# Kernel optimization log

Measured on AMD Instinct MI355X. Metric: run time of the kernel, lower is better.

## Reference

```python
import jax, jax.numpy as jnp
import numpy as np

B, S, D, H, L = 16, 1024, 512, 8, 3
NUM_Q, NUM_C, TOTAL_RES = 10000, 300, 2


def setup_inputs() -> dict:
    k = jax.random.split(jax.random.key(0), 20)
    n = lambda i, s, sc=0.02: jax.random.normal(k[i], s, jnp.float32) * sc
    z = lambda: jnp.zeros((D,), jnp.float32)
    o = lambda: jnp.ones((D,), jnp.float32)
    return {
        'in_ex': jax.random.randint(k[0], (B, S), 0, NUM_Q),
        'in_cat': jax.random.randint(k[1], (B, S), 0, NUM_C),
        'in_res': jax.random.randint(k[2], (B, S), 0, 2),
        'in_pos': n(3, (B, S, D)),
        'en_out': n(4, (B, S, D)),
        'E_res': n(5, (TOTAL_RES + 1, D)),
        'E_ex': n(6, (2 * NUM_Q + 1, D)),
        'E_cat': n(7, (2 * NUM_C + 1, D)),
        'g1': o(), 'be1': z(), 'g2': o(), 'be2': z(), 'g3': o(), 'be3': z(),
        'Wq1': n(8, (D, D)), 'bq1': z(), 'Wk1': n(9, (D, D)), 'bk1': z(),
        'Wv1': n(10, (D, D)), 'bv1': z(), 'Wo1': n(11, (D, D)), 'bo1': z(),
        'Wq2': n(12, (D, D)), 'bq2': z(), 'Wk2': n(13, (D, D)), 'bk2': z(),
        'Wv2': n(14, (D, D)), 'bv2': z(), 'Wo2': n(15, (D, D)), 'bo2': z(),
        'fW1': n(16, (D, D)), 'fb1': z(), 'fW2': n(17, (D, D)), 'fb2': z(),
    }


def layer_norm(x, g, b, eps=1e-5):
    m = x.mean(-1, keepdims=True)
    v = ((x - m) ** 2).mean(-1, keepdims=True)
    return (x - m) / jnp.sqrt(v + eps) * g + b


def pyr_attn(q_in, kv_in, Wq, bq, Wk, bk, Wv, bv, Wo, bo):
    # q_in, kv_in: (S, B, D) as in nn.MultiheadAttention convention
    Sq, Bq, Dm = q_in.shape
    dh = Dm // H
    heads = lambda x: x.reshape(x.shape[0], Bq, H, dh).transpose(1, 2, 0, 3)  # (B,H,S,dh)
    qh = heads(q_in @ Wq + bq)
    kh = heads(kv_in @ Wk + bk)
    vh = heads(kv_in @ Wv + bv)
    Skv = kv_in.shape[0]
    i = jnp.arange(Sq)[:, None]
    Ks, Vs, Ms = [], [], []
    for l in range(L):  # pyramid levels: keys/values avg-pooled by 2**l
        f = 2 ** l
        nb = Skv // f
        Ks.append(kh[:, :, :nb * f].reshape(Bq, H, nb, f, dh).mean(3))
        Vs.append(vh[:, :, :nb * f].reshape(Bq, H, nb, f, dh).mean(3))
        # causal: query i may attend pooled block j only if the block ends at or before i
        Ms.append(i >= (jnp.arange(nb)[None, :] + 1) * f - 1)
    K = jnp.concatenate(Ks, 2)
    V = jnp.concatenate(Vs, 2)
    M = jnp.concatenate(Ms, 1)  # (Sq, K_total) multi-level causal mask
    sc = jnp.einsum('bhqd,bhkd->bhqk', qh, K) / np.sqrt(dh).astype(np.float32)
    sc = jnp.where(M[None, None], sc, -1e9)
    a = jax.nn.softmax(sc, -1)
    out = jnp.einsum('bhqk,bhkd->bhqd', a, V)
    return out.transpose(2, 0, 1, 3).reshape(Sq, Bq, Dm) @ Wo + bo


def reference(in_ex, in_cat, in_res, in_pos, en_out, E_res, E_ex, E_cat,
              g1, be1, g2, be2, g3, be3,
              Wq1, bq1, Wk1, bk1, Wv1, bv1, Wo1, bo1,
              Wq2, bq2, Wk2, bk2, Wv2, bv2, Wo2, bo2,
              fW1, fb1, fW2, fb2):
    # embedding sum (first_block=True)
    out = E_res[in_res] + E_ex[in_ex + NUM_Q * in_res] + E_cat[in_cat + NUM_C * in_res] + in_pos
    out = out.transpose(1, 0, 2)  # (S, B, D)
    out = layer_norm(out, g1, be1)
    out = out + pyr_attn(out, out, Wq1, bq1, Wk1, bk1, Wv1, bv1, Wo1, bo1)
    en = layer_norm(en_out.transpose(1, 0, 2), g2, be2)
    out = out + pyr_attn(out, en, Wq2, bq2, Wk2, bk2, Wv2, bv2, Wo2, bo2)
    out = out.transpose(1, 0, 2)  # (B, S, D)
    out = layer_norm(out, g3, be3)
    out = out + (jax.nn.relu(out @ fW1 + fb1) @ fW2 + fb2)
    return out
```

## Files before the change

### kernel.cpp

```cpp
#include <hip/hip_runtime.h>


#define BB 16
#define SS 1024
#define DD 512
#define HH 8
#define DH 64
#define KTOT 1792
#define NROW (BB*SS)
#define KSW 80

typedef unsigned short u16;
typedef __attribute__((ext_vector_type(8))) u16 u16x8;
typedef __attribute__((ext_vector_type(4))) u16 u16x4;
typedef __attribute__((ext_vector_type(8))) short s16x8;
typedef __attribute__((ext_vector_type(4))) float f32x4;

__device__ __forceinline__ float b2f(u16 u) {
    return __uint_as_float(((unsigned int)u) << 16);
}
__device__ __forceinline__ u16 f2b(float f) {
    unsigned int u = __float_as_uint(f);
    return (u16)((u + 0x7FFF + ((u >> 16) & 1)) >> 16);
}
__device__ __forceinline__ s16x8 u2s8(u16x8 u) {
    union { u16x8 u; s16x8 s; } x; x.u = u; return x.s;
}
__device__ __forceinline__ f32x4 mfma16(s16x8 a, s16x8 b, f32x4 c) {
    return __builtin_amdgcn_mfma_f32_16x16x32_bf16(a, b, c, 0, 0, 0);
}
__device__ __forceinline__ float wave_sum(float v) {
    #pragma unroll
    for (int m = 1; m < 64; m <<= 1) v += __shfl_xor(v, m, 64);
    return v;
}
__device__ __forceinline__ float exp2a(float x) {
    float r;
    asm("v_exp_f32 %0, %1" : "=v"(r) : "v"(x));
    return r;
}
__device__ __forceinline__ unsigned int cvtpk(float a, float b) {
    unsigned int r;
    asm("v_cvt_pk_bf16_f32 %0, %1, %2" : "=v"(r) : "v"(a), "v"(b));
    return r;
}
__device__ __forceinline__ void gl16(const void* g, void* l) {
    __builtin_amdgcn_global_load_lds(
        (const __attribute__((address_space(1))) void*)(unsigned long long)g,
        (__attribute__((address_space(3))) void*)(unsigned int)(unsigned long long)l,
        16, 0, 0);
}

__global__ __launch_bounds__(256) void embed_ln_k(
    const int* __restrict__ in_ex, const int* __restrict__ in_cat,
    const int* __restrict__ in_res, const float* __restrict__ in_pos,
    const float* __restrict__ E_res, const float* __restrict__ E_ex,
    const float* __restrict__ E_cat, const float* __restrict__ g,
    const float* __restrict__ be, float* __restrict__ out)
{
    int wave = threadIdx.x >> 6, lane = threadIdx.x & 63;
    int row = blockIdx.x * 4 + wave;
    int res = in_res[row];
    int ex  = in_ex[row] + 10000 * res;
    int cat = in_cat[row] + 300 * res;
    int d0 = lane * 8;
    const float* pr = &E_res[(size_t)res * DD + d0];
    const float* pe = &E_ex[(size_t)ex * DD + d0];
    const float* pc = &E_cat[(size_t)cat * DD + d0];
    const float* pp = &in_pos[(size_t)row * DD + d0];
    float x[8]; float s = 0.f;
    #pragma unroll
    for (int j = 0; j < 8; j++) { x[j] = pr[j] + pe[j] + pc[j] + pp[j]; s += x[j]; }
    s = wave_sum(s);
    float mean = s * (1.0f / DD);
    float vs = 0.f;
    #pragma unroll
    for (int j = 0; j < 8; j++) { float d = x[j] - mean; vs += d * d; }
    vs = wave_sum(vs);
    float rstd = rsqrtf(vs * (1.0f / DD) + 1e-5f);
    #pragma unroll
    for (int j = 0; j < 8; j++)
        out[(size_t)row * DD + d0 + j] = (x[j] - mean) * rstd * g[d0 + j] + be[d0 + j];
}

template<bool OUTB>
__global__ __launch_bounds__(256) void ln_k(
    const float* __restrict__ x, const float* __restrict__ g,
    const float* __restrict__ be, void* __restrict__ outv)
{
    int wave = threadIdx.x >> 6, lane = threadIdx.x & 63;
    int row = blockIdx.x * 4 + wave;
    int d0 = lane * 8;
    const float* px = &x[(size_t)row * DD + d0];
    float xv[8]; float s = 0.f;
    #pragma unroll
    for (int j = 0; j < 8; j++) { xv[j] = px[j]; s += xv[j]; }
    s = wave_sum(s);
    float mean = s * (1.0f / DD);
    float vs = 0.f;
    #pragma unroll
    for (int j = 0; j < 8; j++) { float d = xv[j] - mean; vs += d * d; }
    vs = wave_sum(vs);
    float rstd = rsqrtf(vs * (1.0f / DD) + 1e-5f);
    #pragma unroll
    for (int j = 0; j < 8; j++) {
        float v = (xv[j] - mean) * rstd * g[d0 + j] + be[d0 + j];
        if (OUTB) ((u16*)outv)[(size_t)row * DD + d0 + j] = f2b(v);
        else      ((float*)outv)[(size_t)row * DD + d0 + j] = v;
    }
}

__global__ __launch_bounds__(256) void transpose_k(const float* __restrict__ src, u16* __restrict__ dst)
{
    int idx = blockIdx.x * 256 + threadIdx.x;
    int n = idx & 511, k = idx >> 9;
    dst[n * 512 + k] = f2b(src[k * 512 + n]);
}

__global__ __launch_bounds__(256) void pool_k12_k(u16* __restrict__ KP)
{
    int idx = blockIdx.x * 256 + threadIdx.x;
    int d = idx & 63;
    int t = idx >> 6;
    int k12 = t % 768;
    int bh = t / 768;
    int s0, f;
    if (k12 < 512) { s0 = 2 * k12; f = 2; } else { s0 = 4 * (k12 - 512); f = 4; }
    size_t base = (size_t)bh * KTOT * DH;
    float acc = 0.f;
    for (int i = 0; i < f; i++)
        acc += b2f(KP[base + (size_t)(s0 + i) * DH + d]);
    KP[base + (size_t)(1024 + k12) * DH + d] = f2b(acc * (1.0f / (float)f));
}

__global__ __launch_bounds__(256) void pool_vt_k(const u16* __restrict__ Vp, u16* __restrict__ VPt)
{
    __shared__ __align__(16) u16 T[64 * 72];
    int tid = threadIdx.x;
    int st = blockIdx.x;
    int h  = blockIdx.y;
    int b  = blockIdx.z;
    int s0 = st * 64;
    {
        const u16* src = &Vp[((size_t)(b * SS + s0)) * DD + h * DH];
        #pragma unroll
        for (int it = 0; it < 2; it++) {
            int idx = it * 256 + tid;
            int row = idx >> 3, unit = idx & 7;
            *(u16x8*)&T[row * 72 + unit * 8] =
                *(const u16x8*)&src[(size_t)row * DD + unit * 8];
        }
    }
    __syncthreads();
    int d = tid & 63, g = tid >> 6;
    size_t obase = ((size_t)(b * HH + h) * DH + d) * KTOT;
    #pragma unroll
    for (int gg = 0; gg < 2; gg++) {
        int grp = g * 2 + gg;
        u16x8 v;
        #pragma unroll
        for (int j = 0; j < 8; j++) v[j] = T[(grp * 8 + j) * 72 + d];
        *(u16x8*)&VPt[obase + s0 + grp * 8] = v;
    }
    {
        u16x8 v;
        #pragma unroll
        for (int j = 0; j < 8; j++) {
            int sl = g * 8 + j;
            float a = b2f(T[(2 * sl) * 72 + d]) + b2f(T[(2 * sl + 1) * 72 + d]);
            v[j] = f2b(a * 0.5f);
        }
        *(u16x8*)&VPt[obase + 1024 + st * 32 + g * 8] = v;
    }
    {
        u16x4 v;
        #pragma unroll
        for (int j = 0; j < 4; j++) {
            int s2 = g * 4 + j;
            float a = 0.f;
            #pragma unroll
            for (int i = 0; i < 4; i++) a += b2f(T[(4 * s2 + i) * 72 + d]);
            v[j] = f2b(a * 0.25f);
        }
        *(u16x4*)&VPt[obase + 1536 + st * 16 + g * 4] = v;
    }
}

template<bool AF32, bool RELU, bool RES, bool OUTB, bool KLAY>
__global__ __launch_bounds__(256) void gemm_k(
    const void* __restrict__ Av, const u16* __restrict__ Wt,
    const float* __restrict__ bias, const float* __restrict__ resid,
    void* __restrict__ Cv, int M, int K, float oscale)
{
    const int N = 512;
    constexpr int ASW = AF32 ? 40 : 32;
    __shared__ __align__(16) u16 As[2][128 * ASW];
    __shared__ __align__(16) u16 Bs[2][128 * 32];
    int tid = threadIdx.x;
    int wave = tid >> 6, lane = tid & 63;
    int quad = lane >> 4, l16 = lane & 15;
    int m0 = blockIdx.y * 128, n0 = blockIdx.x * 128;
    int wm = (wave >> 1) * 64, wn = (wave & 1) * 64;
    int r = tid >> 1, cg = (tid & 1) * 16;
    int grow = wave * 16 + (lane >> 2);
    int gk = (lane & 3) * 8;
    const float* Af = (const float*)Av;
    const u16*  Ab = (const u16*)Av;
    f32x4 acc[4][4];
    #pragma unroll
    for (int i = 0; i < 4; i++)
        #pragma unroll
        for (int j = 0; j < 4; j++)
            #pragma unroll
            for (int rr = 0; rr < 4; rr++) acc[i][j][rr] = 0.f;

    const int NT = K >> 5;
    f32x4 s0, s1, s2, s3;

    #define ISSUE_B(t, buf) { int k0_ = (t) << 5; \
        gl16(&Wt[(size_t)(n0 + grow) * 512 + k0_ + gk],      &Bs[buf][grow * 32 + gk]); \
        gl16(&Wt[(size_t)(n0 + 64 + grow) * 512 + k0_ + gk], &Bs[buf][(64 + grow) * 32 + gk]); }
    #define ISSUE_A16(t, buf) { int k0_ = (t) << 5; \
        gl16(&Ab[(size_t)(m0 + grow) * K + k0_ + gk],      &As[buf][grow * 32 + gk]); \
        gl16(&Ab[(size_t)(m0 + 64 + grow) * K + k0_ + gk], &As[buf][(64 + grow) * 32 + gk]); }
    #define LOAD_A32(t) { const float* src_ = &Af[(size_t)(m0 + r) * K + ((t) << 5) + cg]; \
        s0 = *(const f32x4*)&src_[0];  s1 = *(const f32x4*)&src_[4]; \
        s2 = *(const f32x4*)&src_[8];  s3 = *(const f32x4*)&src_[12]; }
    #define WRITE_A32(buf) { union { unsigned int w[4]; u16x8 v; } L_, H_; \
        L_.w[0] = cvtpk(s0[0], s0[1]); L_.w[1] = cvtpk(s0[2], s0[3]); \
        L_.w[2] = cvtpk(s1[0], s1[1]); L_.w[3] = cvtpk(s1[2], s1[3]); \
        H_.w[0] = cvtpk(s2[0], s2[1]); H_.w[1] = cvtpk(s2[2], s2[3]); \
        H_.w[2] = cvtpk(s3[0], s3[1]); H_.w[3] = cvtpk(s3[2], s3[3]); \
        *(u16x8*)&As[buf][r * ASW + cg]     = L_.v; \
        *(u16x8*)&As[buf][r * ASW + cg + 8] = H_.v; }

    if (AF32) { LOAD_A32(0); WRITE_A32(0); }
    else      { ISSUE_A16(0, 0); }
    ISSUE_B(0, 0);
    __syncthreads();

    for (int t = 0; t < NT; ++t) {
        int cur = t & 1, nxt = cur ^ 1;
        if (t + 1 < NT) {
            if (AF32) { LOAD_A32(t + 1); }
            else      { ISSUE_A16(t + 1, nxt); }
            ISSUE_B(t + 1, nxt);
        }
        s16x8 af[4], bfr[4];
        #pragma unroll
        for (int i = 0; i < 4; i++)
            af[i] = u2s8(*(const u16x8*)&As[cur][(wm + i * 16 + l16) * ASW + quad * 8]);
        #pragma unroll
        for (int j = 0; j < 4; j++)
            bfr[j] = u2s8(*(const u16x8*)&Bs[cur][(wn + j * 16 + l16) * 32 + quad * 8]);
        #pragma unroll
        for (int i = 0; i < 4; i++)
            #pragma unroll
            for (int j = 0; j < 4; j++)
                acc[i][j] = mfma16(af[i], bfr[j], acc[i][j]);
        if (AF32 && t + 1 < NT) { WRITE_A32(nxt); }
        __syncthreads();
    }
    #undef ISSUE_B
    #undef ISSUE_A16
    #undef LOAD_A32
    #undef WRITE_A32

    #pragma unroll
    for (int j = 0; j < 4; j++) {
        int col = n0 + wn + j * 16 + l16;
        float bv = bias[col];
        #pragma unroll
        for (int i = 0; i < 4; i++) {
            int rowb = m0 + wm + i * 16 + quad * 4;
            #pragma unroll
            for (int rr = 0; rr < 4; rr++) {
                float v = (acc[i][j][rr] + bv) * oscale;
                if (RELU) v = fmaxf(v, 0.f);
                int row = rowb + rr;
                if (RES) v += resid[(size_t)row * N + col];
                if (KLAY) {
                    int b_ = row >> 10, s_ = row & 1023;
                    size_t dst = (((size_t)(b_ * HH + (col >> 6)) * KTOT) + s_) * DH + (col & 63);
                    ((u16*)Cv)[dst] = f2b(v);
                } else if (OUTB) {
                    ((u16*)Cv)[(size_t)row * N + col] = f2b(v);
                } else {
                    ((float*)Cv)[(size_t)row * N + col] = v;
                }
            }
        }
    }
}

__global__ __launch_bounds__(256, 2) void attn_k(
    const u16* __restrict__ Qp, const u16* __restrict__ KP,
    const u16* __restrict__ VPt, u16* __restrict__ Hout)
{
    __shared__ __align__(16) u16 Ksh[2][64 * KSW];
    __shared__ __align__(16) u16 Vsh[2][64 * KSW];
    int tid = threadIdx.x;
    int wave = tid >> 6, lane = tid & 63;
    int quad = lane >> 4, l16 = lane & 15;
    int id = blockIdx.x;
    int h = id & 7;
    int inner = id >> 3;
    int x = inner & 3, b = inner >> 2;

    int wx = x * 4 + wave;
    int tiles[4] = { wx, 31 - wx, 32 + wx, 63 - wx };

    const u16* Kb = KP  + ((size_t)(b * HH + h)) * KTOT * DH;
    const u16* Vt = VPt + ((size_t)(b * HH + h)) * DH * KTOT;

    s16x8 qa[4][2];
    f32x4 o[4][4];
    float lrun[4];
    int q0a[4];
    #pragma unroll
    for (int c = 0; c < 4; c++) {
        int q0 = tiles[c] * 16;
        q0a[c] = q0;
        lrun[c] = 0.f;
        const u16* qrow = Qp + ((size_t)(b * SS + q0 + l16)) * DD + h * DH;
        qa[c][0] = u2s8(*(const u16x8*)&qrow[quad * 8]);
        qa[c][1] = u2s8(*(const u16x8*)&qrow[32 + quad * 8]);
        #pragma unroll
        for (int j = 0; j < 4; j++)
            #pragma unroll
            for (int rr = 0; rr < 4; rr++) o[c][j][rr] = 0.f;
    }

    int row0 = 8 * (l16 >> 2) + (l16 & 3);

    int u0 = tid, u1 = 256 + tid;
    int kr0 = u0 >> 3, ku0 = (u0 & 7) * 8;
    int kr1 = u1 >> 3, ku1 = (u1 & 7) * 8;

    u16x8 kreg0 = *(const u16x8*)&Kb[(size_t)u0 * 8];
    u16x8 kreg1 = *(const u16x8*)&Kb[(size_t)u1 * 8];
    u16x8 vreg0 = *(const u16x8*)&Vt[(size_t)kr0 * KTOT + ku0];
    u16x8 vreg1 = *(const u16x8*)&Vt[(size_t)kr1 * KTOT + ku1];
    *(u16x8*)&Ksh[0][kr0 * KSW + ku0] = kreg0;
    *(u16x8*)&Ksh[0][kr1 * KSW + ku1] = kreg1;
    *(u16x8*)&Vsh[0][kr0 * KSW + ku0] = vreg0;
    *(u16x8*)&Vsh[0][kr1 * KSW + ku1] = vreg1;
    __syncthreads();

    for (int ch = 0; ch < 28; ch++) {
        int cur = ch & 1;
        int kbase = ch * 64;
        int lv = (ch < 16) ? 0 : (ch < 24) ? 1 : 2;
        if (ch + 1 < 28) {
            int nb = (ch + 1) * 64;
            kreg0 = *(const u16x8*)&Kb[(size_t)nb * DH + u0 * 8];
            kreg1 = *(const u16x8*)&Kb[(size_t)nb * DH + u1 * 8];
            vreg0 = *(const u16x8*)&Vt[(size_t)kr0 * KTOT + nb + ku0];
            vreg1 = *(const u16x8*)&Vt[(size_t)kr1 * KTOT + nb + ku1];
        }

        int efirst = (lv == 0) ? kbase
                   : (lv == 1) ? 2 * (kbase - 1024) + 1
                               : 4 * (kbase - 1536) + 3;
        int elast  = (lv == 0) ? kbase + 63
                   : (lv == 1) ? 2 * (kbase + 63 - 1024) + 1
                               : 4 * (kbase + 63 - 1536) + 3;
        bool act[4];
        #pragma unroll
        for (int c = 0; c < 4; c++) act[c] = (efirst <= q0a[c] + 15);

        if (act[0] | act[1] | act[2] | act[3]) {
            s16x8 fA[4], fB[4];
            #pragma unroll
            for (int t = 0; t < 4; t++) {
                const int toff = (t & 1) * 4 + (t >> 1) * 32;
                const u16* kr = &Ksh[cur][(row0 + toff) * KSW];
                fA[t] = u2s8(*(const u16x8*)&kr[quad * 8]);
                fB[t] = u2s8(*(const u16x8*)&kr[32 + quad * 8]);
            }
            s16x8 pfa[4], pfb[4];
            #pragma unroll
            for (int c = 0; c < 4; c++) {
                if (!act[c]) continue;
                f32x4 zt[4];
                __builtin_amdgcn_s_setprio(1);
                #pragma unroll
                for (int t = 0; t < 4; t++) {
                    f32x4 z;
                    #pragma unroll
                    for (int rr = 0; rr < 4; rr++) z[rr] = 0.f;
                    z = mfma16(fA[t], qa[c][0], z);
                    zt[t] = mfma16(fB[t], qa[c][1], z);
                }
                __builtin_amdgcn_s_setprio(0);

                if (elast > q0a[c]) {
                    int q = q0a[c] + l16;
                    int kmaxv = (lv == 0) ? q - kbase
                              : (lv == 1) ? ((q - 1) >> 1) - (kbase - 1024)
                                          : ((q - 3) >> 2) - (kbase - 1536);
                    int thrb = kmaxv - 8 * quad;
                    #pragma unroll
                    for (int t = 0; t < 4; t++) {
                        int thr = thrb - ((t & 1) * 4 + (t >> 1) * 32);
                        #pragma unroll
                        for (int rr = 0; rr < 4; rr++)
                            if (rr > thr) zt[t][rr] = -1e30f;
                    }
                }

                float p[4][4]; float ps0 = 0.f, ps1 = 0.f;
                #pragma unroll
                for (int t = 0; t < 4; t++)
                    #pragma unroll
                    for (int rr = 0; rr < 4; rr++) {
                        p[t][rr] = exp2a(zt[t][rr]);
                        if (t & 1) ps1 += p[t][rr]; else ps0 += p[t][rr];
                    }
                float ps = ps0 + ps1;
                ps += __shfl_xor(ps, 16, 64);
                ps += __shfl_xor(ps, 32, 64);
                lrun[c] += ps;

                union { unsigned int w[4]; u16x8 v; } U0, U1;
                U0.w[0] = cvtpk(p[0][0], p[0][1]); U0.w[1] = cvtpk(p[0][2], p[0][3]);
                U0.w[2] = cvtpk(p[1][0], p[1][1]); U0.w[3] = cvtpk(p[1][2], p[1][3]);
                U1.w[0] = cvtpk(p[2][0], p[2][1]); U1.w[1] = cvtpk(p[2][2], p[2][3]);
                U1.w[2] = cvtpk(p[3][0], p[3][1]); U1.w[3] = cvtpk(p[3][2], p[3][3]);
                pfa[c] = u2s8(U0.v); pfb[c] = u2s8(U1.v);
            }

            s16x8 vA[4], vB[4];
            #pragma unroll
            for (int j = 0; j < 4; j++) {
                const u16* vr = &Vsh[cur][(j * 16 + l16) * KSW];
                vA[j] = u2s8(*(const u16x8*)&vr[quad * 8]);
                vB[j] = u2s8(*(const u16x8*)&vr[32 + quad * 8]);
            }
            __builtin_amdgcn_s_setprio(1);
            #pragma unroll
            for (int c = 0; c < 4; c++) {
                if (!act[c]) continue;
                #pragma unroll
                for (int j = 0; j < 4; j++) {
                    o[c][j] = mfma16(pfa[c], vA[j], o[c][j]);
                    o[c][j] = mfma16(pfb[c], vB[j], o[c][j]);
                }
            }
            __builtin_amdgcn_s_setprio(0);
        }

        if (ch + 1 < 28) {
            int nxt = cur ^ 1;
            *(u16x8*)&Ksh[nxt][kr0 * KSW + ku0] = kreg0;
            *(u16x8*)&Ksh[nxt][kr1 * KSW + ku1] = kreg1;
            *(u16x8*)&Vsh[nxt][kr0 * KSW + ku0] = vreg0;
            *(u16x8*)&Vsh[nxt][kr1 * KSW + ku1] = vreg1;
        }
        __syncthreads();
    }

    #pragma unroll
    for (int c = 0; c < 4; c++) {
        float il = 1.0f / lrun[c];
        float ilr[4];
        #pragma unroll
        for (int rr = 0; rr < 4; rr++) ilr[rr] = __shfl(il, quad * 4 + rr, 64);
        #pragma unroll
        for (int rr = 0; rr < 4; rr++) {
            int q = q0a[c] + quad * 4 + rr;
            #pragma unroll
            for (int j = 0; j < 4; j++)
                Hout[((size_t)(b * SS + q)) * DD + h * DH + j * 16 + l16] = f2b(o[c][j][rr] * ilr[rr]);
        }
    }
}

extern "C" void kernel_launch(void* const* d_in, const int* in_sizes, int n_in,
                              void* d_out, int out_size, void* d_ws, size_t ws_size,
                              hipStream_t stream)
{
    (void)in_sizes; (void)n_in; (void)out_size; (void)ws_size;
    const int* in_ex  = (const int*)d_in[0];
    const int* in_cat = (const int*)d_in[1];
    const int* in_res = (const int*)d_in[2];
    const float* in_pos = (const float*)d_in[3];
    const float* en_out = (const float*)d_in[4];
    const float* E_res  = (const float*)d_in[5];
    const float* E_ex   = (const float*)d_in[6];
    const float* E_cat  = (const float*)d_in[7];
    const float* g1 = (const float*)d_in[8],  *be1 = (const float*)d_in[9];
    const float* g2 = (const float*)d_in[10], *be2 = (const float*)d_in[11];
    const float* g3 = (const float*)d_in[12], *be3 = (const float*)d_in[13];
    const float* Wq1 = (const float*)d_in[14], *bq1 = (const float*)d_in[15];
    const float* Wk1 = (const float*)d_in[16], *bk1 = (const float*)d_in[17];
    const float* Wv1 = (const float*)d_in[18], *bv1 = (const float*)d_in[19];
    const float* Wo1 = (const float*)d_in[20], *bo1 = (const float*)d_in[21];
    const float* Wq2 = (const float*)d_in[22], *bq2 = (const float*)d_in[23];
    const float* Wk2 = (const float*)d_in[24], *bk2 = (const float*)d_in[25];
    const float* Wv2 = (const float*)d_in[26], *bv2 = (const float*)d_in[27];
    const float* Wo2 = (const float*)d_in[28], *bo2 = (const float*)d_in[29];
    const float* fW1 = (const float*)d_in[30], *fb1 = (const float*)d_in[31];
    const float* fW2 = (const float*)d_in[32], *fb2 = (const float*)d_in[33];

    char* ws = (char*)d_ws;
    const size_t U = (size_t)NROW * DD * 2;
    float* x1 = (float*)(ws);
    u16* qb   = (u16*)(ws + 2 * U);
    u16* vb   = (u16*)(ws + 3 * U);
    u16* hb   = (u16*)(ws + 4 * U);
    u16* kp   = (u16*)(ws + 5 * U);
    u16* vpt  = (u16*)(ws + 5 * U + 7 * U / 4);
    u16* wt   = (u16*)(ws + 8 * U + U / 2);
    float* x2 = (float*)d_out;
    u16* en = (u16*)(ws);
    float* x3 = x1;
    float* x4 = (float*)(ws + 5 * U);
    u16* ff1 = hb;

    const float* wsrc[10] = {Wq1, Wk1, Wv1, Wo1, Wq2, Wk2, Wv2, Wo2, fW1, fW2};
    for (int i = 0; i < 10; i++)
        transpose_k<<<1024, 256, 0, stream>>>(wsrc[i], wt + (size_t)i * 262144);
    u16* tWq1 = wt,            *tWk1 = wt + 262144,   *tWv1 = wt + 2*262144, *tWo1 = wt + 3*262144;
    u16* tWq2 = wt + 4*262144, *tWk2 = wt + 5*262144, *tWv2 = wt + 6*262144, *tWo2 = wt + 7*262144;
    u16* tF1  = wt + 8*262144, *tF2  = wt + 9*262144;

    dim3 ggrid(4, 128);
    dim3 vtgrid(16, 8, 16);
    const float QSC = 0.18033688f;

    embed_ln_k<<<4096, 256, 0, stream>>>(in_ex, in_cat, in_res, in_pos,
                                         E_res, E_ex, E_cat, g1, be1, x1);

    gemm_k<true,false,false,true,false><<<ggrid, 256, 0, stream>>>(x1, tWq1, bq1, nullptr, qb, NROW, 512, QSC);
    gemm_k<true,false,false,true,true ><<<ggrid, 256, 0, stream>>>(x1, tWk1, bk1, nullptr, kp, NROW, 512, 1.0f);
    gemm_k<true,false,false,true,false><<<ggrid, 256, 0, stream>>>(x1, tWv1, bv1, nullptr, vb, NROW, 512, 1.0f);
    pool_k12_k<<<24576, 256, 0, stream>>>(kp);
    pool_vt_k<<<vtgrid, 256, 0, stream>>>(vb, vpt);
    attn_k<<<512, 256, 0, stream>>>(qb, kp, vpt, hb);
    gemm_k<false,false,true,false,false><<<ggrid, 256, 0, stream>>>(hb, tWo1, bo1, x1, x2, NROW, 512, 1.0f);

    ln_k<true><<<4096, 256, 0, stream>>>(en_out, g2, be2, en);
    gemm_k<true,false,false,true,false><<<ggrid, 256, 0, stream>>>(x2, tWq2, bq2, nullptr, qb, NROW, 512, QSC);
    gemm_k<false,false,false,true,true ><<<ggrid, 256, 0, stream>>>(en, tWk2, bk2, nullptr, kp, NROW, 512, 1.0f);
    gemm_k<false,false,false,true,false><<<ggrid, 256, 0, stream>>>(en, tWv2, bv2, nullptr, vb, NROW, 512, 1.0f);
    pool_k12_k<<<24576, 256, 0, stream>>>(kp);
    pool_vt_k<<<vtgrid, 256, 0, stream>>>(vb, vpt);
    attn_k<<<512, 256, 0, stream>>>(qb, kp, vpt, hb);
    gemm_k<false,false,true,false,false><<<ggrid, 256, 0, stream>>>(hb, tWo2, bo2, x2, x3, NROW, 512, 1.0f);

    ln_k<false><<<4096, 256, 0, stream>>>(x3, g3, be3, x4);
    gemm_k<true,true,false,true,false><<<ggrid, 256, 0, stream>>>(x4, tF1, fb1, nullptr, ff1, NROW, 512, 1.0f);
    gemm_k<false,false,true,false,false><<<ggrid, 256, 0, stream>>>(ff1, tF2, fb2, x4, (float*)d_out, NROW, 512, 1.0f);
}
```

Before: 642.3 us.

## Fuse K pooling into GEMM epilogue, batch weight transposes, split attention finer

The K-projection GEMM epilogue now writes the level-1 and level-2 pooled key rows directly from its four consecutive accumulator rows, which removes the separate pool_k12_k pass (two launches and a re-read of K). The ten per-weight transpose launches become one tiled, LDS-staged transpose kernel that uses vectorized loads and stores. Attention blocks now cover two query tiles per wave instead of four, with double the grid and launch bounds raised to 4 blocks per SM. This improves parallelism and balance but halves K/V tile reuse per block load.

```diff
diff --git a/kernel.cpp b/kernel.cpp
--- a/kernel.cpp
+++ b/kernel.cpp
@@ -110,27 +110,42 @@
     }
 }
 
-__global__ __launch_bounds__(256) void transpose_k(const float* __restrict__ src, u16* __restrict__ dst)
-{
-    int idx = blockIdx.x * 256 + threadIdx.x;
-    int n = idx & 511, k = idx >> 9;
-    dst[n * 512 + k] = f2b(src[k * 512 + n]);
-}
-
-__global__ __launch_bounds__(256) void pool_k12_k(u16* __restrict__ KP)
-{
-    int idx = blockIdx.x * 256 + threadIdx.x;
-    int d = idx & 63;
-    int t = idx >> 6;
-    int k12 = t % 768;
-    int bh = t / 768;
-    int s0, f;
-    if (k12 < 512) { s0 = 2 * k12; f = 2; } else { s0 = 4 * (k12 - 512); f = 4; }
-    size_t base = (size_t)bh * KTOT * DH;
-    float acc = 0.f;
-    for (int i = 0; i < f; i++)
-        acc += b2f(KP[base + (size_t)(s0 + i) * DH + d]);
-    KP[base + (size_t)(1024 + k12) * DH + d] = f2b(acc * (1.0f / (float)f));
+struct W10 { const float* p[10]; };
+__global__ __launch_bounds__(256) void transpose_all_k(W10 wp, u16* __restrict__ dst)
+{
+    __shared__ __align__(16) u16 T[64 * 72];
+    int w = blockIdx.z;
+    const float* src = wp.p[w];
+    u16* d = dst + (size_t)w * 262144;
+    int tk = blockIdx.x;
+    int tn = blockIdx.y;
+    int tid = threadIdx.x;
+    {
+        int r = tid >> 4;
+        int c4 = (tid & 15) * 4;
+        #pragma unroll
+        for (int it = 0; it < 4; it++) {
+            int kr = it * 16 + r;
+            const float* s4 = &src[(size_t)(tk * 64 + kr) * 512 + tn * 64 + c4];
+            f32x4 v = *(const f32x4*)s4;
+            *(unsigned int*)&T[kr * 72 + c4]     = cvtpk(v[0], v[1]);
+            *(unsigned int*)&T[kr * 72 + c4 + 2] = cvtpk(v[2], v[3]);
+        }
+    }
+    __syncthreads();
+    {
+        int nn = tid >> 2;
+        int k16 = (tid & 3) * 16;
+        u16x8 a, b;
+        #pragma unroll
+        for (int j = 0; j < 8; j++) {
+            a[j] = T[(k16 + j) * 72 + nn];
+            b[j] = T[(k16 + 8 + j) * 72 + nn];
+        }
+        u16* o = &d[(size_t)(tn * 64 + nn) * 512 + tk * 64 + k16];
+        *(u16x8*)&o[0] = a;
+        *(u16x8*)&o[8] = b;
+    }
 }
 
 __global__ __launch_bounds__(256) void pool_vt_k(const u16* __restrict__ Vp, u16* __restrict__ VPt)
@@ -273,27 +288,36 @@
         #pragma unroll
         for (int i = 0; i < 4; i++) {
             int rowb = m0 + wm + i * 16 + quad * 4;
-            #pragma unroll
-            for (int rr = 0; rr < 4; rr++) {
-                float v = (acc[i][j][rr] + bv) * oscale;
-                if (RELU) v = fmaxf(v, 0.f);
-                int row = rowb + rr;
-                if (RES) v += resid[(size_t)row * N + col];
-                if (KLAY) {
-                    int b_ = row >> 10, s_ = row & 1023;
-                    size_t dst = (((size_t)(b_ * HH + (col >> 6)) * KTOT) + s_) * DH + (col & 63);
-                    ((u16*)Cv)[dst] = f2b(v);
-                } else if (OUTB) {
-                    ((u16*)Cv)[(size_t)row * N + col] = f2b(v);
-                } else {
-                    ((float*)Cv)[(size_t)row * N + col] = v;
+            if (KLAY) {
+                float vv[4];
+                #pragma unroll
+                for (int rr = 0; rr < 4; rr++) vv[rr] = acc[i][j][rr] + bv;
+                int b_ = rowb >> 10, s_ = rowb & 1023;
+                size_t bh = (size_t)(b_ * HH + (col >> 6)) * KTOT;
+                int dd = col & 63;
+                u16* C16 = (u16*)Cv;
+                #pragma unroll
+                for (int rr = 0; rr < 4; rr++)
+                    C16[(bh + s_ + rr) * DH + dd] = f2b(vv[rr]);
+                C16[(bh + 1024 + (s_ >> 1)) * DH + dd]     = f2b((vv[0] + vv[1]) * 0.5f);
+                C16[(bh + 1024 + (s_ >> 1) + 1) * DH + dd] = f2b((vv[2] + vv[3]) * 0.5f);
+                C16[(bh + 1536 + (s_ >> 2)) * DH + dd]     = f2b((vv[0] + vv[1] + vv[2] + vv[3]) * 0.25f);
+            } else {
+                #pragma unroll
+                for (int rr = 0; rr < 4; rr++) {
+                    float v = (acc[i][j][rr] + bv) * oscale;
+                    if (RELU) v = fmaxf(v, 0.f);
+                    int row = rowb + rr;
+                    if (RES) v += resid[(size_t)row * N + col];
+                    if (OUTB) ((u16*)Cv)[(size_t)row * N + col] = f2b(v);
+                    else      ((float*)Cv)[(size_t)row * N + col] = v;
                 }
             }
         }
     }
 }
 
-__global__ __launch_bounds__(256, 2) void attn_k(
+__global__ __launch_bounds__(256, 4) void attn_k(
     const u16* __restrict__ Qp, const u16* __restrict__ KP,
     const u16* __restrict__ VPt, u16* __restrict__ Hout)
 {
@@ -305,20 +329,20 @@
     int id = blockIdx.x;
     int h = id & 7;
     int inner = id >> 3;
-    int x = inner & 3, b = inner >> 2;
-
-    int wx = x * 4 + wave;
-    int tiles[4] = { wx, 31 - wx, 32 + wx, 63 - wx };
+    int x = inner & 7, b = inner >> 3;
+
+    int wg = x * 4 + wave;
+    int tiles[2] = { wg, 63 - wg };
 
     const u16* Kb = KP  + ((size_t)(b * HH + h)) * KTOT * DH;
     const u16* Vt = VPt + ((size_t)(b * HH + h)) * DH * KTOT;
 
-    s16x8 qa[4][2];
-    f32x4 o[4][4];
-    float lrun[4];
-    int q0a[4];
-    #pragma unroll
-    for (int c = 0; c < 4; c++) {
+    s16x8 qa[2][2];
+    f32x4 o[2][4];
+    float lrun[2];
+    int q0a[2];
+    #pragma unroll
+    for (int c = 0; c < 2; c++) {
         int q0 = tiles[c] * 16;
         q0a[c] = q0;
         lrun[c] = 0.f;
@@ -365,11 +389,11 @@
         int elast  = (lv == 0) ? kbase + 63
                    : (lv == 1) ? 2 * (kbase + 63 - 1024) + 1
                                : 4 * (kbase + 63 - 1536) + 3;
-        bool act[4];
-        #pragma unroll
-        for (int c = 0; c < 4; c++) act[c] = (efirst <= q0a[c] + 15);
-
-        if (act[0] | act[1] | act[2] | act[3]) {
+        bool act[2];
+        #pragma unroll
+        for (int c = 0; c < 2; c++) act[c] = (efirst <= q0a[c] + 15);
+
+        if (act[0] | act[1]) {
             s16x8 fA[4], fB[4];
             #pragma unroll
             for (int t = 0; t < 4; t++) {
@@ -378,9 +402,9 @@
                 fA[t] = u2s8(*(const u16x8*)&kr[quad * 8]);
                 fB[t] = u2s8(*(const u16x8*)&kr[32 + quad * 8]);
             }
-            s16x8 pfa[4], pfb[4];
-            #pragma unroll
-            for (int c = 0; c < 4; c++) {
+            s16x8 pfa[2], pfb[2];
+            #pragma unroll
+            for (int c = 0; c < 2; c++) {
                 if (!act[c]) continue;
                 f32x4 zt[4];
                 __builtin_amdgcn_s_setprio(1);
@@ -439,7 +463,7 @@
             }
             __builtin_amdgcn_s_setprio(1);
             #pragma unroll
-            for (int c = 0; c < 4; c++) {
+            for (int c = 0; c < 2; c++) {
                 if (!act[c]) continue;
                 #pragma unroll
                 for (int j = 0; j < 4; j++) {
@@ -461,7 +485,7 @@
     }
 
     #pragma unroll
-    for (int c = 0; c < 4; c++) {
+    for (int c = 0; c < 2; c++) {
         float il = 1.0f / lrun[c];
         float ilr[4];
         #pragma unroll
@@ -518,9 +542,10 @@
     float* x4 = (float*)(ws + 5 * U);
     u16* ff1 = hb;
 
+    W10 wp;
     const float* wsrc[10] = {Wq1, Wk1, Wv1, Wo1, Wq2, Wk2, Wv2, Wo2, fW1, fW2};
-    for (int i = 0; i < 10; i++)
-        transpose_k<<<1024, 256, 0, stream>>>(wsrc[i], wt + (size_t)i * 262144);
+    for (int i = 0; i < 10; i++) wp.p[i] = wsrc[i];
+    transpose_all_k<<<dim3(8, 8, 10), 256, 0, stream>>>(wp, wt);
     u16* tWq1 = wt,            *tWk1 = wt + 262144,   *tWv1 = wt + 2*262144, *tWo1 = wt + 3*262144;
     u16* tWq2 = wt + 4*262144, *tWk2 = wt + 5*262144, *tWv2 = wt + 6*262144, *tWo2 = wt + 7*262144;
     u16* tF1  = wt + 8*262144, *tF2  = wt + 9*262144;
@@ -535,18 +560,16 @@
     gemm_k<true,false,false,true,false><<<ggrid, 256, 0, stream>>>(x1, tWq1, bq1, nullptr, qb, NROW, 512, QSC);
     gemm_k<true,false,false,true,true ><<<ggrid, 256, 0, stream>>>(x1, tWk1, bk1, nullptr, kp, NROW, 512, 1.0f);
     gemm_k<true,false,false,true,false><<<ggrid, 256, 0, stream>>>(x1, tWv1, bv1, nullptr, vb, NROW, 512, 1.0f);
-    pool_k12_k<<<24576, 256, 0, stream>>>(kp);
     pool_vt_k<<<vtgrid, 256, 0, stream>>>(vb, vpt);
-    attn_k<<<512, 256, 0, stream>>>(qb, kp, vpt, hb);
+    attn_k<<<1024, 256, 0, stream>>>(qb, kp, vpt, hb);
     gemm_k<false,false,true,false,false><<<ggrid, 256, 0, stream>>>(hb, tWo1, bo1, x1, x2, NROW, 512, 1.0f);
 
     ln_k<true><<<4096, 256, 0, stream>>>(en_out, g2, be2, en);
     gemm_k<true,false,false,true,false><<<ggrid, 256, 0, stream>>>(x2, tWq2, bq2, nullptr, qb, NROW, 512, QSC);
     gemm_k<false,false,false,true,true ><<<ggrid, 256, 0, stream>>>(en, tWk2, bk2, nullptr, kp, NROW, 512, 1.0f);
     gemm_k<false,false,false,true,false><<<ggrid, 256, 0, stream>>>(en, tWv2, bv2, nullptr, vb, NROW, 512, 1.0f);
-    pool_k12_k<<<24576, 256, 0, stream>>>(kp);
     pool_vt_k<<<vtgrid, 256, 0, stream>>>(vb, vpt);
-    attn_k<<<512, 256, 0, stream>>>(qb, kp, vpt, hb);
+    attn_k<<<1024, 256, 0, stream>>>(qb, kp, vpt, hb);
     gemm_k<false,false,true,false,false><<<ggrid, 256, 0, stream>>>(hb, tWo2, bo2, x2, x3, NROW, 512, 1.0f);
 
     ln_k<false><<<4096, 256, 0, stream>>>(x3, g3, be3, x4);
```

After: 709.7 us. 10.5% more time.
